# Optimization experiments

Measured on AMD Instinct MI355X. Metric: run time of the kernel, lower is better.

The kernel has to match this reference:

```python
import jax, jax.numpy as jnp
import numpy as np

N_NODES = 100000
N_EDGES = 1600000
N_GRAPHS = 256
HID = 128
NCLS = 3
NEG_SLOPE = 0.2  # DGL GATConv default leaky_relu slope


def gat_layer(h, src, dst, W, al, ar, b):
    # h: [N, Din] -> z: [N, H]
    z = h @ W
    el = z @ al  # [N] attention logits (left / source term)
    er = z @ ar  # [N] attention logits (right / dest term)
    e = jax.nn.leaky_relu(el[src] + er[dst], NEG_SLOPE)  # [E]
    # edge softmax normalized over incoming edges of each dst node
    m = jax.ops.segment_max(e, dst, num_segments=N_NODES)  # [N]
    ex = jnp.exp(e - m[dst])
    s = jax.ops.segment_sum(ex, dst, num_segments=N_NODES)  # [N]
    alpha = ex / jnp.maximum(s[dst], 1e-9)  # [E]
    # scatter-aggregate weighted source features to dst
    out = jax.ops.segment_sum(alpha[:, None] * z[src], dst, num_segments=N_NODES)
    return out + b  # [N, H]


def setup_inputs() -> dict:
    key = jax.random.key(0)
    ks = jax.random.split(key, 16)
    edge_src = jax.random.randint(ks[0], (N_EDGES,), 0, N_NODES)
    edge_dst = jax.random.randint(ks[1], (N_EDGES,), 0, N_NODES)
    graph_ids = jnp.sort(jax.random.randint(ks[2], (N_NODES,), 0, N_GRAPHS))
    sc = 0.1
    return {
        "edge_src": edge_src,
        "edge_dst": edge_dst,
        "graph_ids": graph_ids,
        "W1": jax.random.normal(ks[3], (1, HID), jnp.float32) * sc,
        "al1": jax.random.normal(ks[4], (HID,), jnp.float32) * sc,
        "ar1": jax.random.normal(ks[5], (HID,), jnp.float32) * sc,
        "b1": jax.random.normal(ks[6], (HID,), jnp.float32) * sc,
        "W2": jax.random.normal(ks[7], (HID, HID), jnp.float32) * sc,
        "al2": jax.random.normal(ks[8], (HID,), jnp.float32) * sc,
        "ar2": jax.random.normal(ks[9], (HID,), jnp.float32) * sc,
        "b2": jax.random.normal(ks[10], (HID,), jnp.float32) * sc,
        "Wc": jax.random.normal(ks[11], (HID, NCLS), jnp.float32) * sc,
        "bc": jax.random.normal(ks[12], (NCLS,), jnp.float32) * sc,
    }


def reference(edge_src, edge_dst, graph_ids, W1, al1, ar1, b1, W2, al2, ar2, b2, Wc, bc):
    # initial node features = in-degree, shape [N, 1]
    indeg = jax.ops.segment_sum(jnp.ones((N_EDGES,), jnp.float32), edge_dst,
                                num_segments=N_NODES)
    h = indeg[:, None]
    h = jax.nn.elu(gat_layer(h, edge_src, edge_dst, W1, al1, ar1, b1))
    h = jax.nn.elu(gat_layer(h, edge_src, edge_dst, W2, al2, ar2, b2))
    # dgl.mean_nodes: per-graph mean readout
    sums = jax.ops.segment_sum(h, graph_ids, num_segments=N_GRAPHS)  # [G, H]
    cnts = jax.ops.segment_sum(jnp.ones((N_NODES,), jnp.float32), graph_ids,
                               num_segments=N_GRAPHS)
    hg = sums / jnp.maximum(cnts, 1.0)[:, None]
    return hg @ Wc + bc  # [G, num_classes]
```

## Files before the change

### kernel.cpp

```cpp
#include <hip/hip_runtime.h>
#include <cstdint>
#include <cstddef>

#define N_NODES 100000
#define N_EDGES 1600000
#define N_GRAPHS 256
#define HID 128
#define NCLASS 8

#define SCHUNK 2048
#define SNB ((N_NODES + SCHUNK - 1) / SCHUNK)

static __device__ __forceinline__ float lrelu(float x) { return x >= 0.f ? x : 0.2f * x; }
static __device__ __forceinline__ float elu_f(float x) { return x > 0.f ? x : expm1f(x); }
static __device__ __forceinline__ unsigned f2bf(float x) {
    union { float f; unsigned u; } v; v.f = x;
    return (v.u + 0x7FFFu + ((v.u >> 16) & 1u)) >> 16;
}
static __device__ __forceinline__ float bf_lo(unsigned u) { return __uint_as_float(u << 16); }
static __device__ __forceinline__ float bf_hi(unsigned u) { return __uint_as_float(u & 0xFFFF0000u); }

__global__ void k_prep(const float* __restrict__ W1, const float* __restrict__ al1,
                       const float* __restrict__ ar1, float* __restrict__ scal) {
    int l = threadIdx.x;
    float pl = W1[l] * al1[l] + W1[l + 64] * al1[l + 64];
    float pr = W1[l] * ar1[l] + W1[l + 64] * ar1[l + 64];
    for (int m = 32; m >= 1; m >>= 1) { pl += __shfl_xor(pl, m); pr += __shfl_xor(pr, m); }
    if (l == 0) { scal[0] = pl; scal[1] = pr; }
}

__global__ void k_degrank(const int* __restrict__ dst, int* __restrict__ dr,
                          int* __restrict__ rank) {
    int i = blockIdx.x * blockDim.x + threadIdx.x;
    int st = gridDim.x * blockDim.x;
    for (; i < N_EDGES; i += st) {
        int cls = (i >> 8) & (NCLASS - 1);
        rank[i] = atomicAdd(&dr[cls * N_NODES + dst[i]], 1);
    }
}

__global__ void k_sum(const int* __restrict__ dr, int* __restrict__ deg) {
    int d = blockIdx.x * blockDim.x + threadIdx.x;
    if (d < N_NODES) {
        int s = 0;
#pragma unroll
        for (int r = 0; r < NCLASS; r++) s += dr[r * N_NODES + d];
        deg[d] = s;
    }
}

__global__ void k_scan_part(const int* __restrict__ deg, int* __restrict__ P) {
    __shared__ int sh[256];
    int base = blockIdx.x * SCHUNK + threadIdx.x * 8;
    int s = 0;
#pragma unroll
    for (int e = 0; e < 8; e++) { int idx = base + e; if (idx < N_NODES) s += deg[idx]; }
    sh[threadIdx.x] = s; __syncthreads();
    for (int d = 128; d >= 1; d >>= 1) {
        if (threadIdx.x < d) sh[threadIdx.x] += sh[threadIdx.x + d];
        __syncthreads();
    }
    if (threadIdx.x == 0) P[blockIdx.x] = sh[0];
}

__global__ void k_scan_p2(const int* __restrict__ P, int* __restrict__ P2, int* __restrict__ offs) {
    if (threadIdx.x == 0) {
        int run = 0;
        for (int b = 0; b < SNB; b++) { P2[b] = run; run += P[b]; }
        offs[N_NODES] = run;
    }
}

__global__ void k_scan_final(const int* __restrict__ deg, const int* __restrict__ P2,
                             int* __restrict__ offs) {
    __shared__ int sh[256];
    int base = blockIdx.x * SCHUNK + threadIdx.x * 8;
    int loc[8]; int s = 0;
#pragma unroll
    for (int e = 0; e < 8; e++) {
        int idx = base + e;
        loc[e] = (idx < N_NODES) ? deg[idx] : 0;
        s += loc[e];
    }
    int own = s;
    sh[threadIdx.x] = s; __syncthreads();
    for (int d = 1; d < 256; d <<= 1) {
        int v = (threadIdx.x >= (unsigned)d) ? sh[threadIdx.x - d] : 0;
        __syncthreads();
        sh[threadIdx.x] += v;
        __syncthreads();
    }
    int run = P2[blockIdx.x] + sh[threadIdx.x] - own;
#pragma unroll
    for (int e = 0; e < 8; e++) {
        int idx = base + e;
        if (idx < N_NODES) { offs[idx] = run; run += loc[e]; }
    }
}

__global__ void k_base(const int* __restrict__ dr, const int* __restrict__ offs,
                       int* __restrict__ base) {
    int d = blockIdx.x * blockDim.x + threadIdx.x;
    if (d < N_NODES) {
        int run = offs[d];
#pragma unroll
        for (int r = 0; r < NCLASS; r++) { base[r * N_NODES + d] = run; run += dr[r * N_NODES + d]; }
    }
}

__global__ void k_fill(const int* __restrict__ src, const int* __restrict__ dst,
                       const int* __restrict__ base, const int* __restrict__ rank,
                       int* __restrict__ csr) {
    int i = blockIdx.x * blockDim.x + threadIdx.x;
    int st = gridDim.x * blockDim.x;
    for (; i < N_EDGES; i += st) {
        int cls = (i >> 8) & (NCLASS - 1);
        int pos = base[cls * N_NODES + dst[i]] + rank[i];
        csr[pos] = src[i];
    }
}

__global__ __launch_bounds__(256) void k_l1(const int* __restrict__ deg, const int* __restrict__ offs,
                                            const int* __restrict__ csr_src, const float* __restrict__ scal,
                                            float* __restrict__ t) {
    int node = blockIdx.x * 4 + (threadIdx.x >> 6);
    if (node >= N_NODES) return;
    int l = threadIdx.x & 63;
    float cl = scal[0], cr = scal[1];
    float eri = cr * (float)deg[node];
    int off = offs[node], end = offs[node + 1];
    float m = -INFINITY, den = 0.f, num = 0.f;
    for (int e = off + l; e < end; e += 64) {
        int s = csr_src[e];
        float ds = (float)deg[s];
        float e1 = lrelu(cl * ds + eri);
        if (e1 > m) { float c = __expf(m - e1); den *= c; num *= c; m = e1; }
        float w = __expf(e1 - m);
        den += w; num += w * ds;
    }
    for (int st = 1; st < 64; st <<= 1) {
        float mo = __shfl_xor(m, st);
        float dn = __shfl_xor(den, st);
        float no = __shfl_xor(num, st);
        float mn = fmaxf(m, mo);
        float sa = (m  > -1e37f) ? __expf(m  - mn) : 0.f;
        float sb = (mo > -1e37f) ? __expf(mo - mn) : 0.f;
        den = den * sa + dn * sb;
        num = num * sa + no * sb;
        m = mn;
    }
    if (l == 0) t[node] = num / fmaxf(den, 1e-9f);
}

__global__ __launch_bounds__(256, 2) void k_gemm(
    const float* __restrict__ t, const float* __restrict__ W1, const float* __restrict__ b1,
    const float* __restrict__ W2, const float* __restrict__ al2, const float* __restrict__ ar2,
    unsigned* __restrict__ zb, float* __restrict__ el2, float* __restrict__ er2) {
    __shared__ float h1s[8][8][HID];
    __shared__ float W1s[HID], b1s[HID], al2s[HID], ar2s[HID];
    if (threadIdx.x < HID) {
        W1s[threadIdx.x] = W1[threadIdx.x]; b1s[threadIdx.x] = b1[threadIdx.x];
        al2s[threadIdx.x] = al2[threadIdx.x]; ar2s[threadIdx.x] = ar2[threadIdx.x];
    }
    __syncthreads();
    int g = threadIdx.x >> 5;
    int lt = threadIdx.x & 31;
    const float4* W2v = (const float4*)W2;
    for (int i0 = blockIdx.x * 64; i0 < N_NODES; i0 += gridDim.x * 64) {
        int ibase = i0 + g * 8;
        for (int n = 0; n < 8; n++) {
            int i = ibase + n;
            if (i < N_NODES) {
                float ti = t[i];
                float4 hv;
                hv.x = elu_f(ti * W1s[4 * lt + 0] + b1s[4 * lt + 0]);
                hv.y = elu_f(ti * W1s[4 * lt + 1] + b1s[4 * lt + 1]);
                hv.z = elu_f(ti * W1s[4 * lt + 2] + b1s[4 * lt + 2]);
                hv.w = elu_f(ti * W1s[4 * lt + 3] + b1s[4 * lt + 3]);
                *(float4*)&h1s[g][n][4 * lt] = hv;
            }
        }
        __syncthreads();
        float4 acc[8];
#pragma unroll
        for (int n = 0; n < 8; n++) acc[n] = make_float4(0.f, 0.f, 0.f, 0.f);
#pragma unroll 4
        for (int k = 0; k < HID; k++) {
            float4 w = W2v[k * 32 + lt];
#pragma unroll
            for (int n = 0; n < 8; n++) {
                float h = h1s[g][n][k];
                acc[n].x += h * w.x; acc[n].y += h * w.y;
                acc[n].z += h * w.z; acc[n].w += h * w.w;
            }
        }
#pragma unroll
        for (int n = 0; n < 8; n++) {
            int i = ibase + n;
            if (i < N_NODES) {
                float4 a = acc[n];
                uint2 st;
                st.x = f2bf(a.x) | (f2bf(a.y) << 16);
                st.y = f2bf(a.z) | (f2bf(a.w) << 16);
                *(uint2*)&zb[(size_t)i * 64 + 2 * lt] = st;
                float pl = a.x * al2s[4 * lt] + a.y * al2s[4 * lt + 1] +
                           a.z * al2s[4 * lt + 2] + a.w * al2s[4 * lt + 3];
                float pr = a.x * ar2s[4 * lt] + a.y * ar2s[4 * lt + 1] +
                           a.z * ar2s[4 * lt + 2] + a.w * ar2s[4 * lt + 3];
                for (int mm = 16; mm >= 1; mm >>= 1) { pl += __shfl_xor(pl, mm); pr += __shfl_xor(pr, mm); }
                if (lt == 0) { el2[i] = pl; er2[i] = pr; }
            }
        }
        __syncthreads();
    }
}

__global__ __launch_bounds__(256) void k_att2(
    const int* __restrict__ offs, const int* __restrict__ csr_src,
    const float* __restrict__ el2, const float* __restrict__ er2,
    float* __restrict__ alpha) {
    int node = blockIdx.x * 4 + (threadIdx.x >> 6);
    if (node >= N_NODES) return;
    int l = threadIdx.x & 63;
    float eri = er2[node];
    int off = offs[node], end = offs[node + 1];
    float m = -INFINITY, den = 0.f;
    for (int e = off + l; e < end; e += 64) {
        int s = csr_src[e];
        float x = el2[s] + eri;
        float e2 = x >= 0.f ? x : 0.2f * x;
        if (e2 > m) { den *= __expf(m - e2); m = e2; }
        den += __expf(e2 - m);
    }
    for (int st = 1; st < 64; st <<= 1) {
        float mo = __shfl_xor(m, st);
        float dn = __shfl_xor(den, st);
        float mn = fmaxf(m, mo);
        float sa = (m  > -1e37f) ? __expf(m  - mn) : 0.f;
        float sb = (mo > -1e37f) ? __expf(mo - mn) : 0.f;
        den = den * sa + dn * sb;
        m = mn;
    }
    float rden = 1.f / fmaxf(den, 1e-9f);
    for (int e = off + l; e < end; e += 64) {
        int s = csr_src[e];
        float x = el2[s] + eri;
        float e2 = x >= 0.f ? x : 0.2f * x;
        alpha[e] = __expf(e2 - m) * rden;
    }
}

__global__ __launch_bounds__(256) void k_agg2(
    const int* __restrict__ offs, const int* __restrict__ csr_src,
    const float* __restrict__ alpha, const unsigned* __restrict__ zb,
    const float* __restrict__ b2, float* __restrict__ h2) {
    int node = blockIdx.x * 4 + (threadIdx.x >> 6);
    if (node >= N_NODES) return;
    int l = threadIdx.x & 63;
    int off = offs[node], end = offs[node + 1];
    float a0 = 0.f, a1 = 0.f;
    int e = off;
    for (; e + 4 <= end; e += 4) {
        int s0 = csr_src[e], s1 = csr_src[e + 1], s2 = csr_src[e + 2], s3 = csr_src[e + 3];
        float w0 = alpha[e], w1 = alpha[e + 1], w2 = alpha[e + 2], w3 = alpha[e + 3];
        unsigned z0 = zb[(size_t)s0 * 64 + l];
        unsigned z1 = zb[(size_t)s1 * 64 + l];
        unsigned z2 = zb[(size_t)s2 * 64 + l];
        unsigned z3 = zb[(size_t)s3 * 64 + l];
        a0 += w0 * bf_lo(z0) + w1 * bf_lo(z1) + w2 * bf_lo(z2) + w3 * bf_lo(z3);
        a1 += w0 * bf_hi(z0) + w1 * bf_hi(z1) + w2 * bf_hi(z2) + w3 * bf_hi(z3);
    }
    for (; e < end; e++) {
        int s = csr_src[e];
        float w = alpha[e];
        unsigned z = zb[(size_t)s * 64 + l];
        a0 += w * bf_lo(z);
        a1 += w * bf_hi(z);
    }
    float2 bb = *(const float2*)&b2[2 * l];
    float2 o;
    o.x = elu_f(a0 + bb.x);
    o.y = elu_f(a1 + bb.y);
    *(float2*)&h2[(size_t)node * HID + 2 * l] = o;
}

static __device__ __forceinline__ int lower_bound_i(const int* a, int n, int v) {
    int lo = 0, hi = n;
    while (lo < hi) { int mid = (lo + hi) >> 1; if (a[mid] < v) lo = mid + 1; else hi = mid; }
    return lo;
}

__global__ __launch_bounds__(1024) void k_pool(const int* __restrict__ gids, const float* __restrict__ h2,
                                               const float* __restrict__ Wc, const float* __restrict__ bc,
                                               float* __restrict__ out) {
    int g = blockIdx.x;
    int lo = lower_bound_i(gids, N_NODES, g);
    int hi = lower_bound_i(gids, N_NODES, g + 1);
    int j = threadIdx.x & 127;
    int nn = threadIdx.x >> 7;
    float s = 0.f;
    for (int n = lo + nn; n < hi; n += 8) s += h2[(size_t)n * HID + j];
    __shared__ float red[1024];
    red[threadIdx.x] = s;
    __syncthreads();
    __shared__ float red2[2][3];
    if (threadIdx.x < 128) {
        float hg = 0.f;
#pragma unroll
        for (int q = 0; q < 8; q++) hg += red[q * 128 + j];
        hg /= fmaxf((float)(hi - lo), 1.f);
        float p0 = hg * Wc[j * 3 + 0];
        float p1 = hg * Wc[j * 3 + 1];
        float p2 = hg * Wc[j * 3 + 2];
        for (int mm = 32; mm >= 1; mm >>= 1) {
            p0 += __shfl_xor(p0, mm); p1 += __shfl_xor(p1, mm); p2 += __shfl_xor(p2, mm);
        }
        if ((threadIdx.x & 63) == 0) {
            int w = threadIdx.x >> 6;
            red2[w][0] = p0; red2[w][1] = p1; red2[w][2] = p2;
        }
    }
    __syncthreads();
    if (threadIdx.x < 3)
        out[g * 3 + threadIdx.x] = red2[0][threadIdx.x] + red2[1][threadIdx.x] + bc[threadIdx.x];
}

extern "C" void kernel_launch(void* const* d_in, const int* in_sizes, int n_in,
                              void* d_out, int out_size, void* d_ws, size_t ws_size,
                              hipStream_t stream) {
    (void)in_sizes; (void)n_in; (void)out_size; (void)ws_size;
    const int* edge_src = (const int*)d_in[0];
    const int* edge_dst = (const int*)d_in[1];
    const int* gids     = (const int*)d_in[2];
    const float* W1  = (const float*)d_in[3];
    const float* al1 = (const float*)d_in[4];
    const float* ar1 = (const float*)d_in[5];
    const float* b1  = (const float*)d_in[6];
    const float* W2  = (const float*)d_in[7];
    const float* al2 = (const float*)d_in[8];
    const float* ar2 = (const float*)d_in[9];
    const float* b2  = (const float*)d_in[10];
    const float* Wc  = (const float*)d_in[11];
    const float* bc  = (const float*)d_in[12];
    float* out = (float*)d_out;

    char* p = (char*)d_ws;
    auto alloc = [&](size_t bytes) -> char* {
        char* r = p;
        p += (bytes + 511) & ~(size_t)511;
        return r;
    };
    int*      dr    = (int*)alloc((size_t)NCLASS * N_NODES * 4);
    int*      base  = (int*)alloc((size_t)NCLASS * N_NODES * 4);
    int*      rank  = (int*)alloc((size_t)N_EDGES * 4);
    int*      offs  = (int*)alloc((size_t)(N_NODES + 1) * 4);
    int*      P     = (int*)alloc((size_t)SNB * 4);
    int*      P2    = (int*)alloc((size_t)SNB * 4);
    float*    scal  = (float*)alloc(64);
    int*      csr   = (int*)alloc((size_t)N_EDGES * 4);
    int*      deg   = (int*)alloc((size_t)N_NODES * 4);
    float*    t     = (float*)alloc((size_t)N_NODES * 4);
    float*    el2   = (float*)alloc((size_t)N_NODES * 4);
    float*    er2   = (float*)alloc((size_t)N_NODES * 4);
    unsigned* zb    = (unsigned*)alloc((size_t)N_NODES * 64 * 4);
    float*    h2    = (float*)alloc((size_t)N_NODES * HID * 4);
    float*    al_e  = (float*)rank;

    hipMemsetAsync(dr, 0, (size_t)NCLASS * N_NODES * 4, stream);

    k_prep<<<1, 64, 0, stream>>>(W1, al1, ar1, scal);
    k_degrank<<<2048, 256, 0, stream>>>(edge_dst, dr, rank);
    k_sum<<<(N_NODES + 255) / 256, 256, 0, stream>>>(dr, deg);
    k_scan_part<<<SNB, 256, 0, stream>>>(deg, P);
    k_scan_p2<<<1, 64, 0, stream>>>(P, P2, offs);
    k_scan_final<<<SNB, 256, 0, stream>>>(deg, P2, offs);
    k_base<<<(N_NODES + 255) / 256, 256, 0, stream>>>(dr, offs, base);
    k_fill<<<2048, 256, 0, stream>>>(edge_src, edge_dst, base, rank, csr);
    k_l1<<<(N_NODES + 3) / 4, 256, 0, stream>>>(deg, offs, csr, scal, t);
    k_gemm<<<(N_NODES + 63) / 64, 256, 0, stream>>>(t, W1, b1, W2, al2, ar2, zb, el2, er2);
    k_att2<<<(N_NODES + 3) / 4, 256, 0, stream>>>(offs, csr, el2, er2, al_e);
    k_agg2<<<(N_NODES + 3) / 4, 256, 0, stream>>>(offs, csr, al_e, zb, b2, h2);
    k_pool<<<N_GRAPHS, 1024, 0, stream>>>(gids, h2, Wc, bc, out);
}
```

Baseline: 403.8 us.

## Fuse layer-2 attention and aggregation; vectorize GEMM inner loop over k

Merges the attention-softmax kernel and the aggregation kernel into one. The per-edge alpha is now recomputed inline from el2 and er2 during aggregation instead of being written to and read back from a global array. This removes one launch and an edge-sized write/read, at the cost of redundant exp and el2 gathers across all 64 lanes. The GEMM kernel also reads four k-steps of h from shared memory as float4 and raises the launch_bounds occupancy hint from 2 to 4, which risks register pressure.

```diff
diff --git a/kernel.cpp b/kernel.cpp
--- a/kernel.cpp
+++ b/kernel.cpp
@@ -152,7 +152,7 @@
     if (l == 0) t[node] = num / fmaxf(den, 1e-9f);
 }
 
-__global__ __launch_bounds__(256, 2) void k_gemm(
+__global__ __launch_bounds__(256, 4) void k_gemm(
     const float* __restrict__ t, const float* __restrict__ W1, const float* __restrict__ b1,
     const float* __restrict__ W2, const float* __restrict__ al2, const float* __restrict__ ar2,
     unsigned* __restrict__ zb, float* __restrict__ el2, float* __restrict__ er2) {
@@ -184,14 +184,18 @@
         float4 acc[8];
 #pragma unroll
         for (int n = 0; n < 8; n++) acc[n] = make_float4(0.f, 0.f, 0.f, 0.f);
-#pragma unroll 4
-        for (int k = 0; k < HID; k++) {
-            float4 w = W2v[k * 32 + lt];
+        for (int j = 0; j < HID / 4; j++) {
+            float4 w0 = W2v[(4 * j + 0) * 32 + lt];
+            float4 w1 = W2v[(4 * j + 1) * 32 + lt];
+            float4 w2 = W2v[(4 * j + 2) * 32 + lt];
+            float4 w3 = W2v[(4 * j + 3) * 32 + lt];
 #pragma unroll
             for (int n = 0; n < 8; n++) {
-                float h = h1s[g][n][k];
-                acc[n].x += h * w.x; acc[n].y += h * w.y;
-                acc[n].z += h * w.z; acc[n].w += h * w.w;
+                float4 hv = *(const float4*)&h1s[g][n][4 * j];
+                acc[n].x += hv.x * w0.x + hv.y * w1.x + hv.z * w2.x + hv.w * w3.x;
+                acc[n].y += hv.x * w0.y + hv.y * w1.y + hv.z * w2.y + hv.w * w3.y;
+                acc[n].z += hv.x * w0.z + hv.y * w1.z + hv.z * w2.z + hv.w * w3.z;
+                acc[n].w += hv.x * w0.w + hv.y * w1.w + hv.z * w2.w + hv.w * w3.w;
             }
         }
 #pragma unroll
@@ -215,10 +219,11 @@
     }
 }
 
-__global__ __launch_bounds__(256) void k_att2(
+__global__ __launch_bounds__(256) void k_l2f(
     const int* __restrict__ offs, const int* __restrict__ csr_src,
     const float* __restrict__ el2, const float* __restrict__ er2,
-    float* __restrict__ alpha) {
+    const unsigned* __restrict__ zb, const float* __restrict__ b2,
+    float* __restrict__ h2) {
     int node = blockIdx.x * 4 + (threadIdx.x >> 6);
     if (node >= N_NODES) return;
     int l = threadIdx.x & 63;
@@ -242,27 +247,15 @@
         m = mn;
     }
     float rden = 1.f / fmaxf(den, 1e-9f);
-    for (int e = off + l; e < end; e += 64) {
-        int s = csr_src[e];
-        float x = el2[s] + eri;
-        float e2 = x >= 0.f ? x : 0.2f * x;
-        alpha[e] = __expf(e2 - m) * rden;
-    }
-}
-
-__global__ __launch_bounds__(256) void k_agg2(
-    const int* __restrict__ offs, const int* __restrict__ csr_src,
-    const float* __restrict__ alpha, const unsigned* __restrict__ zb,
-    const float* __restrict__ b2, float* __restrict__ h2) {
-    int node = blockIdx.x * 4 + (threadIdx.x >> 6);
-    if (node >= N_NODES) return;
-    int l = threadIdx.x & 63;
-    int off = offs[node], end = offs[node + 1];
     float a0 = 0.f, a1 = 0.f;
     int e = off;
     for (; e + 4 <= end; e += 4) {
         int s0 = csr_src[e], s1 = csr_src[e + 1], s2 = csr_src[e + 2], s3 = csr_src[e + 3];
-        float w0 = alpha[e], w1 = alpha[e + 1], w2 = alpha[e + 2], w3 = alpha[e + 3];
+        float x0 = el2[s0] + eri, x1 = el2[s1] + eri, x2 = el2[s2] + eri, x3 = el2[s3] + eri;
+        float w0 = __expf(lrelu(x0) - m) * rden;
+        float w1 = __expf(lrelu(x1) - m) * rden;
+        float w2 = __expf(lrelu(x2) - m) * rden;
+        float w3 = __expf(lrelu(x3) - m) * rden;
         unsigned z0 = zb[(size_t)s0 * 64 + l];
         unsigned z1 = zb[(size_t)s1 * 64 + l];
         unsigned z2 = zb[(size_t)s2 * 64 + l];
@@ -272,7 +265,8 @@
     }
     for (; e < end; e++) {
         int s = csr_src[e];
-        float w = alpha[e];
+        float x = el2[s] + eri;
+        float w = __expf(lrelu(x) - m) * rden;
         unsigned z = zb[(size_t)s * 64 + l];
         a0 += w * bf_lo(z);
         a1 += w * bf_hi(z);
@@ -364,7 +358,6 @@
     float*    er2   = (float*)alloc((size_t)N_NODES * 4);
     unsigned* zb    = (unsigned*)alloc((size_t)N_NODES * 64 * 4);
     float*    h2    = (float*)alloc((size_t)N_NODES * HID * 4);
-    float*    al_e  = (float*)rank;
 
     hipMemsetAsync(dr, 0, (size_t)NCLASS * N_NODES * 4, stream);
 
@@ -378,7 +371,6 @@
     k_fill<<<2048, 256, 0, stream>>>(edge_src, edge_dst, base, rank, csr);
     k_l1<<<(N_NODES + 3) / 4, 256, 0, stream>>>(deg, offs, csr, scal, t);
     k_gemm<<<(N_NODES + 63) / 64, 256, 0, stream>>>(t, W1, b1, W2, al2, ar2, zb, el2, er2);
-    k_att2<<<(N_NODES + 3) / 4, 256, 0, stream>>>(offs, csr, el2, er2, al_e);
-    k_agg2<<<(N_NODES + 3) / 4, 256, 0, stream>>>(offs, csr, al_e, zb, b2, h2);
+    k_l2f<<<(N_NODES + 3) / 4, 256, 0, stream>>>(offs, csr, el2, er2, zb, b2, h2);
     k_pool<<<N_GRAPHS, 1024, 0, stream>>>(gids, h2, Wc, bc, out);
 }
```

New measurement: 404.2 us. About the same (+0.1%).
